# Kernel tuning notes

Hardware: AMD Instinct MI355X
Metric: run time of the kernel (lower is better)

Reference implementation:

```python
import jax, jax.numpy as jnp
import numpy as np

B, S, D = 4, 2048, 512
H, DK, DV = 8, 64, 64
EPS = 1e-6
MASK_FILL = -1e-9  # faithful to the original masked_fill value (NOT -inf)


def setup_inputs() -> dict:
    key = jax.random.key(0)
    ks = jax.random.split(key, 9)
    sc = 0.05
    return {
        "q": jax.random.normal(ks[0], (B, S, D), jnp.float32),
        "k": jax.random.normal(ks[1], (B, S, D), jnp.float32),
        "v": jax.random.normal(ks[2], (B, S, D), jnp.float32),
        "src_mask": jax.random.randint(ks[3], (B, S), 0, 2, jnp.int32),
        "Wq": jax.random.normal(ks[4], (D, H * DK), jnp.float32) * sc,
        "Wk": jax.random.normal(ks[5], (D, H * DK), jnp.float32) * sc,
        "Wv": jax.random.normal(ks[6], (D, H * DV), jnp.float32) * sc,
        "Wo": jax.random.normal(ks[7], (H * DV, D), jnp.float32) * sc,
        "gamma": jnp.ones((D,), jnp.float32),
        "beta": jnp.zeros((D,), jnp.float32),
    }


def reference(q, k, v, src_mask, Wq, Wk, Wv, Wo, gamma, beta):
    b, len_q, _ = q.shape
    residual = q
    # QKV projections -> [B, H, S, dk/dv]
    qh = (q @ Wq).reshape(b, len_q, H, DK).transpose(0, 2, 1, 3)
    kh = (k @ Wk).reshape(b, -1, H, DK).transpose(0, 2, 1, 3)
    vh = (v @ Wv).reshape(b, -1, H, DV).transpose(0, 2, 1, 3)
    # scores [B, H, S, S]
    attn = jnp.einsum('bhqd,bhkd->bhqk', qh, kh) / jnp.sqrt(jnp.float32(DK))
    # pairwise src mask: outer product of [B,S] mask, diagonal forced to 1
    sm = src_mask[:, :len_q].astype(jnp.float32)
    am = sm[:, :, None] * sm[:, None, :]               # [B, S, S]
    idx = jnp.arange(len_q)
    am = am.at[:, idx, idx].set(1.0)
    attn = jnp.where(am[:, None, :, :] == 0, MASK_FILL, attn)
    attn = jax.nn.softmax(attn, axis=-1)
    out = jnp.einsum('bhqk,bhkd->bhqd', attn, vh)      # [B, H, S, dv]
    out = out.transpose(0, 2, 1, 3).reshape(b, len_q, H * DV)
    out = out @ Wo + residual
    # LayerNorm(eps=1e-6)
    mu = jnp.mean(out, axis=-1, keepdims=True)
    var = jnp.var(out, axis=-1, keepdims=True)
    out = (out - mu) * jax.lax.rsqrt(var + EPS) * gamma + beta
    return out, attn
```

## Files before the change

### kernel.cpp

```cpp
#include <hip/hip_runtime.h>
#include <math.h>

#define B_ 4
#define S_ 2048
#define D_ 512
#define H_ 8
#define NEG_FILL (-1e-9f)

typedef __attribute__((ext_vector_type(8))) short bf16x8;
typedef __attribute__((ext_vector_type(4))) float f32x4;

#define MFMA16(A, Bm, C) __builtin_amdgcn_mfma_f32_16x16x32_bf16((A), (Bm), (C), 0, 0, 0)

__device__ __forceinline__ short f2b(float f) {
  union { float f; unsigned u; } x;
  x.f = f;
  unsigned r = x.u + 0x7fffu + ((x.u >> 16) & 1u);
  return (short)(r >> 16);
}

__global__ __launch_bounds__(256) void prep_wt(
    const float* __restrict__ Wq, const float* __restrict__ Wk,
    const float* __restrict__ Wv, const float* __restrict__ Wo,
    short* __restrict__ Wqt, short* __restrict__ Wkt,
    short* __restrict__ Wvt, short* __restrict__ Wot)
{
  const float* W; short* Wt;
  switch (blockIdx.z) {
    case 0: W = Wq; Wt = Wqt; break;
    case 1: W = Wk; Wt = Wkt; break;
    case 2: W = Wv; Wt = Wvt; break;
    default: W = Wo; Wt = Wot; break;
  }
  __shared__ float Ws[64 * 68];
  const int t = threadIdx.x;
  const int n0 = blockIdx.x * 64, k0 = blockIdx.y * 64;

  #pragma unroll
  for (int rep = 0; rep < 4; ++rep) {
    int e4 = rep * 256 + t;
    int r = e4 >> 4, c0 = (e4 & 15) * 4;
    *(float4*)&Ws[r * 68 + c0] = *(const float4*)&W[(size_t)(k0 + r) * 512 + n0 + c0];
  }
  __syncthreads();

  int rn = t >> 2;
  int kb = (t & 3) * 16;
  union { short s[8]; int4 v; } pk;
  #pragma unroll
  for (int half = 0; half < 2; ++half) {
    #pragma unroll
    for (int i = 0; i < 8; ++i)
      pk.s[i] = f2b(Ws[(kb + half * 8 + i) * 68 + rn]);
    *(int4*)&Wt[(size_t)(n0 + rn) * 512 + k0 + kb + half * 8] = pk.v;
  }
}

__global__ __launch_bounds__(256) void qkv_mfma(
    const float* __restrict__ q, const float* __restrict__ k, const float* __restrict__ v,
    const short* __restrict__ Wqt, const short* __restrict__ Wkt, const short* __restrict__ Wvt,
    short* __restrict__ qh, short* __restrict__ kh, short* __restrict__ vt)
{
  const int z = blockIdx.z;
  const float* X = (z == 0) ? q : (z == 1) ? k : v;
  const short* Wt = (z == 0) ? Wqt : (z == 1) ? Wkt : Wvt;

  __shared__ short Xs[64 * 72];
  __shared__ short Wsh[64 * 72];

  const int t = threadIdx.x;
  const int wave = t >> 6, lane = t & 63, quad = lane >> 4, l15 = lane & 15;
  const int tile_n = blockIdx.x * 64;
  const int tile_m = blockIdx.y * 64;

  f32x4 acc[4];
  #pragma unroll
  for (int nt = 0; nt < 4; ++nt) acc[nt] = (f32x4){0.f, 0.f, 0.f, 0.f};

  for (int k0 = 0; k0 < 512; k0 += 64) {
    __syncthreads();
    #pragma unroll
    for (int rep = 0; rep < 4; ++rep) {
      int e4 = rep * 256 + t;
      int row = e4 >> 4, c0 = (e4 & 15) * 4;
      float4 xv = *(const float4*)&X[(size_t)(tile_m + row) * 512 + k0 + c0];
      *(short4*)&Xs[row * 72 + c0] =
          make_short4(f2b(xv.x), f2b(xv.y), f2b(xv.z), f2b(xv.w));
    }
    #pragma unroll
    for (int rep = 0; rep < 2; ++rep) {
      int e = rep * 256 + t;
      int row = e >> 3, c0 = (e & 7) * 8;
      *(int4*)&Wsh[row * 72 + c0] = *(const int4*)&Wt[(size_t)(tile_n + row) * 512 + k0 + c0];
    }
    __syncthreads();
    #pragma unroll
    for (int ks = 0; ks < 2; ++ks) {
      bf16x8 af = *(bf16x8*)&Xs[(wave * 16 + l15) * 72 + ks * 32 + quad * 8];
      #pragma unroll
      for (int nt = 0; nt < 4; ++nt) {
        bf16x8 bfr = *(bf16x8*)&Wsh[(nt * 16 + l15) * 72 + ks * 32 + quad * 8];
        acc[nt] = MFMA16(af, bfr, acc[nt]);
      }
    }
  }

  const int h = tile_n >> 6;
  if (z < 2) {
    short* Y = (z == 0) ? qh : kh;
    #pragma unroll
    for (int nt = 0; nt < 4; ++nt) {
      int d = nt * 16 + l15;
      #pragma unroll
      for (int r = 0; r < 4; ++r) {
        int row = tile_m + wave * 16 + quad * 4 + r;
        int b = row >> 11, s = row & (S_ - 1);
        Y[(((size_t)(b * H_ + h)) * S_ + s) * 64 + d] = f2b(acc[nt][r]);
      }
    }
  } else {
    int row0 = tile_m + wave * 16 + quad * 4;
    int b = row0 >> 11, s0 = row0 & (S_ - 1);
    #pragma unroll
    for (int nt = 0; nt < 4; ++nt) {
      int d = nt * 16 + l15;
      short4 pk = make_short4(f2b(acc[nt][0]), f2b(acc[nt][1]),
                              f2b(acc[nt][2]), f2b(acc[nt][3]));
      *(short4*)&vt[(((size_t)(b * H_ + h)) * 64 + d) * S_ + s0] = pk;
    }
  }
}

__global__ __launch_bounds__(256) void attn_mfma(
    const short* __restrict__ qh, const short* __restrict__ kh,
    const short* __restrict__ vt, const int* __restrict__ src_mask,
    float* __restrict__ attn_out, short* __restrict__ ohb)
{
  const int t = threadIdx.x;
  const int wave = t >> 6, lane = t & 63, quad = lane >> 4, l15 = lane & 15;
  const int q0 = blockIdx.x * 64;
  const int bh = blockIdx.y, b = bh >> 3, h = bh & 7;

  __shared__ short Ks[64 * 72];
  __shared__ short Vs[64 * 72];
  __shared__ short Ps[64 * 72];
  __shared__ int smq[64], smk[64];

  #pragma unroll
  for (int rep = 0; rep < 2; ++rep) {
    int e = rep * 256 + t;
    int row = e >> 3, c0 = (e & 7) * 8;
    *(int4*)&Ps[row * 72 + c0] =
        *(const int4*)&qh[((size_t)bh * S_ + q0 + row) * 64 + c0];
  }
  if (t < 64) smq[t] = src_mask[b * S_ + q0 + t];
  __syncthreads();

  bf16x8 qf[2];
  #pragma unroll
  for (int ks = 0; ks < 2; ++ks)
    qf[ks] = *(bf16x8*)&Ps[(wave * 16 + l15) * 72 + ks * 32 + quad * 8];

  int rloc[4], mqr[4], qir[4];
  #pragma unroll
  for (int r = 0; r < 4; ++r) {
    rloc[r] = wave * 16 + quad * 4 + r;
    mqr[r] = smq[rloc[r]];
    qir[r] = q0 + rloc[r];
  }

  float rs[4] = {0.f, 0.f, 0.f, 0.f};
  for (int kt0 = 0; kt0 < S_; kt0 += 64) {
    __syncthreads();
    #pragma unroll
    for (int rep = 0; rep < 2; ++rep) {
      int e = rep * 256 + t;
      int row = e >> 3, c0 = (e & 7) * 8;
      *(int4*)&Ks[row * 72 + c0] =
          *(const int4*)&kh[((size_t)bh * S_ + kt0 + row) * 64 + c0];
    }
    if (t < 64) smk[t] = src_mask[b * S_ + kt0 + t];
    __syncthreads();

    #pragma unroll
    for (int nt = 0; nt < 4; ++nt) {
      f32x4 c = (f32x4){0.f, 0.f, 0.f, 0.f};
      #pragma unroll
      for (int ks = 0; ks < 2; ++ks) {
        bf16x8 kf = *(bf16x8*)&Ks[(nt * 16 + l15) * 72 + ks * 32 + quad * 8];
        c = MFMA16(qf[ks], kf, c);
      }
      int mk = smk[nt * 16 + l15];
      int kj = kt0 + nt * 16 + l15;
      #pragma unroll
      for (int r = 0; r < 4; ++r) {
        float ss = c[r] * 0.125f;
        bool keep = (mqr[r] & mk) || (qir[r] == kj);
        ss = keep ? ss : NEG_FILL;
        rs[r] += __expf(ss);
      }
    }
  }
  #pragma unroll
  for (int r = 0; r < 4; ++r) {
    float vsum = rs[r];
    vsum += __shfl_xor(vsum, 1);
    vsum += __shfl_xor(vsum, 2);
    vsum += __shfl_xor(vsum, 4);
    vsum += __shfl_xor(vsum, 8);
    rs[r] = 1.f / vsum;
  }

  f32x4 oacc[4];
  #pragma unroll
  for (int dt = 0; dt < 4; ++dt) oacc[dt] = (f32x4){0.f, 0.f, 0.f, 0.f};

  for (int kt0 = 0; kt0 < S_; kt0 += 64) {
    __syncthreads();
    #pragma unroll
    for (int rep = 0; rep < 2; ++rep) {
      int e = rep * 256 + t;
      int row = e >> 3, c0 = (e & 7) * 8;
      *(int4*)&Ks[row * 72 + c0] =
          *(const int4*)&kh[((size_t)bh * S_ + kt0 + row) * 64 + c0];
      *(int4*)&Vs[row * 72 + c0] =
          *(const int4*)&vt[((size_t)bh * 64 + row) * S_ + kt0 + c0];
    }
    if (t < 64) smk[t] = src_mask[b * S_ + kt0 + t];
    __syncthreads();

    #pragma unroll
    for (int nt = 0; nt < 4; ++nt) {
      f32x4 c = (f32x4){0.f, 0.f, 0.f, 0.f};
      #pragma unroll
      for (int ks = 0; ks < 2; ++ks) {
        bf16x8 kf = *(bf16x8*)&Ks[(nt * 16 + l15) * 72 + ks * 32 + quad * 8];
        c = MFMA16(qf[ks], kf, c);
      }
      int mk = smk[nt * 16 + l15];
      int kj = kt0 + nt * 16 + l15;
      #pragma unroll
      for (int r = 0; r < 4; ++r) {
        float ss = c[r] * 0.125f;
        bool keep = (mqr[r] & mk) || (qir[r] == kj);
        ss = keep ? ss : NEG_FILL;
        float p = __expf(ss) * rs[r];
        attn_out[((size_t)bh * S_ + q0 + rloc[r]) * S_ + kj] = p;
        Ps[rloc[r] * 72 + nt * 16 + l15] = f2b(p);
      }
    }
    __syncthreads();

    bf16x8 pf[2];
    #pragma unroll
    for (int ks = 0; ks < 2; ++ks)
      pf[ks] = *(bf16x8*)&Ps[(wave * 16 + l15) * 72 + ks * 32 + quad * 8];
    #pragma unroll
    for (int dt = 0; dt < 4; ++dt) {
      #pragma unroll
      for (int ks = 0; ks < 2; ++ks) {
        bf16x8 vf = *(bf16x8*)&Vs[(dt * 16 + l15) * 72 + ks * 32 + quad * 8];
        oacc[dt] = MFMA16(pf[ks], vf, oacc[dt]);
      }
    }
  }

  #pragma unroll
  for (int dt = 0; dt < 4; ++dt) {
    int d = h * 64 + dt * 16 + l15;
    #pragma unroll
    for (int r = 0; r < 4; ++r)
      ohb[((size_t)b * S_ + q0 + rloc[r]) * 512 + d] = f2b(oacc[dt][r]);
  }
}

__global__ __launch_bounds__(256) void out_mfma(
    const short* __restrict__ ohb, const short* __restrict__ Wot,
    const float* __restrict__ resid, float* __restrict__ out)
{
  __shared__ short Xs[64 * 72];
  __shared__ short Wsh[64 * 72];

  const int t = threadIdx.x;
  const int wave = t >> 6, lane = t & 63, quad = lane >> 4, l15 = lane & 15;
  const int tile_n = blockIdx.x * 64;
  const int tile_m = blockIdx.y * 64;

  f32x4 acc[4];
  #pragma unroll
  for (int nt = 0; nt < 4; ++nt) acc[nt] = (f32x4){0.f, 0.f, 0.f, 0.f};

  for (int k0 = 0; k0 < 512; k0 += 64) {
    __syncthreads();
    #pragma unroll
    for (int rep = 0; rep < 2; ++rep) {
      int e = rep * 256 + t;
      int row = e >> 3, c0 = (e & 7) * 8;
      *(int4*)&Xs[row * 72 + c0] = *(const int4*)&ohb[(size_t)(tile_m + row) * 512 + k0 + c0];
      *(int4*)&Wsh[row * 72 + c0] = *(const int4*)&Wot[(size_t)(tile_n + row) * 512 + k0 + c0];
    }
    __syncthreads();
    #pragma unroll
    for (int ks = 0; ks < 2; ++ks) {
      bf16x8 af = *(bf16x8*)&Xs[(wave * 16 + l15) * 72 + ks * 32 + quad * 8];
      #pragma unroll
      for (int nt = 0; nt < 4; ++nt) {
        bf16x8 bfr = *(bf16x8*)&Wsh[(nt * 16 + l15) * 72 + ks * 32 + quad * 8];
        acc[nt] = MFMA16(af, bfr, acc[nt]);
      }
    }
  }

  #pragma unroll
  for (int nt = 0; nt < 4; ++nt) {
    int c = tile_n + nt * 16 + l15;
    #pragma unroll
    for (int r = 0; r < 4; ++r) {
      size_t row = tile_m + wave * 16 + quad * 4 + r;
      out[row * 512 + c] = acc[nt][r] + resid[row * 512 + c];
    }
  }
}

__global__ __launch_bounds__(256) void ln_kernel(
    float* __restrict__ io, const float* __restrict__ gamma, const float* __restrict__ beta)
{
  const int wid  = threadIdx.x >> 6;
  const int lane = threadIdx.x & 63;
  const size_t row = (size_t)blockIdx.x * 4 + wid;
  const size_t base = row * 512 + lane * 8;

  float4 x0 = *(const float4*)&io[base];
  float4 x1 = *(const float4*)&io[base + 4];
  float xs[8] = {x0.x, x0.y, x0.z, x0.w, x1.x, x1.y, x1.z, x1.w};

  float s = 0.f, s2 = 0.f;
  #pragma unroll
  for (int i = 0; i < 8; ++i) { s += xs[i]; s2 = fmaf(xs[i], xs[i], s2); }
  #pragma unroll
  for (int m = 1; m < 64; m <<= 1) {
    s  += __shfl_xor(s, m);
    s2 += __shfl_xor(s2, m);
  }
  float mu  = s * (1.f / 512.f);
  float var = s2 * (1.f / 512.f) - mu * mu;
  float rsq = rsqrtf(var + 1e-6f);

  float4 g0 = *(const float4*)&gamma[lane * 8];
  float4 g1 = *(const float4*)&gamma[lane * 8 + 4];
  float4 b0 = *(const float4*)&beta[lane * 8];
  float4 b1 = *(const float4*)&beta[lane * 8 + 4];
  float gs[8] = {g0.x, g0.y, g0.z, g0.w, g1.x, g1.y, g1.z, g1.w};
  float bs[8] = {b0.x, b0.y, b0.z, b0.w, b1.x, b1.y, b1.z, b1.w};

  float ys[8];
  #pragma unroll
  for (int i = 0; i < 8; ++i) ys[i] = (xs[i] - mu) * rsq * gs[i] + bs[i];
  *(float4*)&io[base]     = make_float4(ys[0], ys[1], ys[2], ys[3]);
  *(float4*)&io[base + 4] = make_float4(ys[4], ys[5], ys[6], ys[7]);
}

extern "C" void kernel_launch(void* const* d_in, const int* in_sizes, int n_in,
                              void* d_out, int out_size, void* d_ws, size_t ws_size,
                              hipStream_t stream)
{
  const float* q     = (const float*)d_in[0];
  const float* k     = (const float*)d_in[1];
  const float* v     = (const float*)d_in[2];
  const int*  smask  = (const int*)d_in[3];
  const float* Wq    = (const float*)d_in[4];
  const float* Wk    = (const float*)d_in[5];
  const float* Wv    = (const float*)d_in[6];
  const float* Wo    = (const float*)d_in[7];
  const float* gamma = (const float*)d_in[8];
  const float* beta  = (const float*)d_in[9];

  float* out  = (float*)d_out;
  float* attn = out + (size_t)B_ * S_ * D_;

  short* wsS = (short*)d_ws;
  short* qh  = wsS;
  short* kh  = qh + 4194304;
  short* vt  = kh + 4194304;
  short* ohb = vt + 4194304;
  short* Wqt = ohb + 4194304;
  short* Wkt = Wqt + 262144;
  short* Wvt = Wkt + 262144;
  short* Wot = Wvt + 262144;

  prep_wt<<<dim3(8, 8, 4), 256, 0, stream>>>(Wq, Wk, Wv, Wo, Wqt, Wkt, Wvt, Wot);
  qkv_mfma<<<dim3(8, 128, 3), 256, 0, stream>>>(q, k, v, Wqt, Wkt, Wvt, qh, kh, vt);
  attn_mfma<<<dim3(32, 32), 256, 0, stream>>>(qh, kh, vt, smask, attn, ohb);
  out_mfma<<<dim3(8, 128), 256, 0, stream>>>(ohb, Wot, q, out);
  ln_kernel<<<2048, 256, 0, stream>>>(out, gamma, beta);
}
```

Measured before the change: 804.3 us.

## Simplify attention masking arithmetically, fold score scale into Q, widen GEMM tiles

```diff
diff --git a/kernel.cpp b/kernel.cpp
--- a/kernel.cpp
+++ b/kernel.cpp
@@ -5,7 +5,6 @@
 #define S_ 2048
 #define D_ 512
 #define H_ 8
-#define NEG_FILL (-1e-9f)
 
 typedef __attribute__((ext_vector_type(8))) short bf16x8;
 typedef __attribute__((ext_vector_type(4))) float f32x4;
@@ -66,16 +65,16 @@
   const short* Wt = (z == 0) ? Wqt : (z == 1) ? Wkt : Wvt;
 
   __shared__ short Xs[64 * 72];
-  __shared__ short Wsh[64 * 72];
+  __shared__ short Wsh[128 * 72];
 
   const int t = threadIdx.x;
   const int wave = t >> 6, lane = t & 63, quad = lane >> 4, l15 = lane & 15;
-  const int tile_n = blockIdx.x * 64;
+  const int tile_n = blockIdx.x * 128;
   const int tile_m = blockIdx.y * 64;
 
-  f32x4 acc[4];
-  #pragma unroll
-  for (int nt = 0; nt < 4; ++nt) acc[nt] = (f32x4){0.f, 0.f, 0.f, 0.f};
+  f32x4 acc[8];
+  #pragma unroll
+  for (int nt = 0; nt < 8; ++nt) acc[nt] = (f32x4){0.f, 0.f, 0.f, 0.f};
 
   for (int k0 = 0; k0 < 512; k0 += 64) {
     __syncthreads();
@@ -88,7 +87,7 @@
           make_short4(f2b(xv.x), f2b(xv.y), f2b(xv.z), f2b(xv.w));
     }
     #pragma unroll
-    for (int rep = 0; rep < 2; ++rep) {
+    for (int rep = 0; rep < 4; ++rep) {
       int e = rep * 256 + t;
       int row = e >> 3, c0 = (e & 7) * 8;
       *(int4*)&Wsh[row * 72 + c0] = *(const int4*)&Wt[(size_t)(tile_n + row) * 512 + k0 + c0];
@@ -98,35 +97,37 @@
     for (int ks = 0; ks < 2; ++ks) {
       bf16x8 af = *(bf16x8*)&Xs[(wave * 16 + l15) * 72 + ks * 32 + quad * 8];
       #pragma unroll
-      for (int nt = 0; nt < 4; ++nt) {
+      for (int nt = 0; nt < 8; ++nt) {
         bf16x8 bfr = *(bf16x8*)&Wsh[(nt * 16 + l15) * 72 + ks * 32 + quad * 8];
         acc[nt] = MFMA16(af, bfr, acc[nt]);
       }
     }
   }
 
-  const int h = tile_n >> 6;
+  const float scale = (z == 0) ? 0.125f : 1.0f;
   if (z < 2) {
     short* Y = (z == 0) ? qh : kh;
     #pragma unroll
-    for (int nt = 0; nt < 4; ++nt) {
-      int d = nt * 16 + l15;
+    for (int nt = 0; nt < 8; ++nt) {
+      int d = tile_n + nt * 16 + l15;
+      int h = d >> 6, dd = d & 63;
       #pragma unroll
       for (int r = 0; r < 4; ++r) {
         int row = tile_m + wave * 16 + quad * 4 + r;
         int b = row >> 11, s = row & (S_ - 1);
-        Y[(((size_t)(b * H_ + h)) * S_ + s) * 64 + d] = f2b(acc[nt][r]);
+        Y[(((size_t)(b * H_ + h)) * S_ + s) * 64 + dd] = f2b(acc[nt][r] * scale);
       }
     }
   } else {
     int row0 = tile_m + wave * 16 + quad * 4;
     int b = row0 >> 11, s0 = row0 & (S_ - 1);
     #pragma unroll
-    for (int nt = 0; nt < 4; ++nt) {
-      int d = nt * 16 + l15;
+    for (int nt = 0; nt < 8; ++nt) {
+      int d = tile_n + nt * 16 + l15;
+      int h = d >> 6, dd = d & 63;
       short4 pk = make_short4(f2b(acc[nt][0]), f2b(acc[nt][1]),
                               f2b(acc[nt][2]), f2b(acc[nt][3]));
-      *(short4*)&vt[(((size_t)(b * H_ + h)) * 64 + d) * S_ + s0] = pk;
+      *(short4*)&vt[(((size_t)(b * H_ + h)) * 64 + dd) * S_ + s0] = pk;
     }
   }
 }
@@ -144,7 +145,7 @@
   __shared__ short Ks[64 * 72];
   __shared__ short Vs[64 * 72];
   __shared__ short Ps[64 * 72];
-  __shared__ int smq[64], smk[64];
+  __shared__ float smqf[64], smkf[64];
 
   #pragma unroll
   for (int rep = 0; rep < 2; ++rep) {
@@ -153,7 +154,7 @@
     *(int4*)&Ps[row * 72 + c0] =
         *(const int4*)&qh[((size_t)bh * S_ + q0 + row) * 64 + c0];
   }
-  if (t < 64) smq[t] = src_mask[b * S_ + q0 + t];
+  if (t < 64) smqf[t] = (float)src_mask[b * S_ + q0 + t];
   __syncthreads();
 
   bf16x8 qf[2];
@@ -161,15 +162,15 @@
   for (int ks = 0; ks < 2; ++ks)
     qf[ks] = *(bf16x8*)&Ps[(wave * 16 + l15) * 72 + ks * 32 + quad * 8];
 
-  int rloc[4], mqr[4], qir[4];
+  int rloc[4];
+  float mqf[4];
   #pragma unroll
   for (int r = 0; r < 4; ++r) {
     rloc[r] = wave * 16 + quad * 4 + r;
-    mqr[r] = smq[rloc[r]];
-    qir[r] = q0 + rloc[r];
-  }
-
-  float rs[4] = {0.f, 0.f, 0.f, 0.f};
+    mqf[r] = smqf[rloc[r]];
+  }
+
+  float rs[4] = {128.f, 128.f, 128.f, 128.f};
   for (int kt0 = 0; kt0 < S_; kt0 += 64) {
     __syncthreads();
     #pragma unroll
@@ -179,9 +180,10 @@
       *(int4*)&Ks[row * 72 + c0] =
           *(const int4*)&kh[((size_t)bh * S_ + kt0 + row) * 64 + c0];
     }
-    if (t < 64) smk[t] = src_mask[b * S_ + kt0 + t];
-    __syncthreads();
-
+    if (t < 64) smkf[t] = (float)src_mask[b * S_ + kt0 + t];
+    __syncthreads();
+
+    const bool diagtile = (kt0 == q0);
     #pragma unroll
     for (int nt = 0; nt < 4; ++nt) {
       f32x4 c = (f32x4){0.f, 0.f, 0.f, 0.f};
@@ -190,14 +192,23 @@
         bf16x8 kf = *(bf16x8*)&Ks[(nt * 16 + l15) * 72 + ks * 32 + quad * 8];
         c = MFMA16(qf[ks], kf, c);
       }
-      int mk = smk[nt * 16 + l15];
-      int kj = kt0 + nt * 16 + l15;
-      #pragma unroll
-      for (int r = 0; r < 4; ++r) {
-        float ss = c[r] * 0.125f;
-        bool keep = (mqr[r] & mk) || (qir[r] == kj);
-        ss = keep ? ss : NEG_FILL;
-        rs[r] += __expf(ss);
+      float mk = smkf[nt * 16 + l15];
+      if (diagtile && nt == wave) {
+        #pragma unroll
+        for (int r = 0; r < 4; ++r) {
+          float e = __expf(c[r]);
+          float mm = mqf[r] * mk;
+          float pun = fmaf(mm, e - 1.f, 1.f);
+          if (l15 == quad * 4 + r) pun = e;
+          rs[r] += pun - 1.f;
+        }
+      } else {
+        #pragma unroll
+        for (int r = 0; r < 4; ++r) {
+          float e = __expf(c[r]);
+          float mm = mqf[r] * mk;
+          rs[r] = fmaf(mm, e - 1.f, rs[r]);
+        }
       }
     }
   }
@@ -215,6 +226,11 @@
   #pragma unroll
   for (int dt = 0; dt < 4; ++dt) oacc[dt] = (f32x4){0.f, 0.f, 0.f, 0.f};
 
+  float* arow[4];
+  #pragma unroll
+  for (int r = 0; r < 4; ++r)
+    arow[r] = attn_out + ((size_t)bh * S_ + q0 + rloc[r]) * S_;
+
   for (int kt0 = 0; kt0 < S_; kt0 += 64) {
     __syncthreads();
     #pragma unroll
@@ -226,9 +242,10 @@
       *(int4*)&Vs[row * 72 + c0] =
           *(const int4*)&vt[((size_t)bh * 64 + row) * S_ + kt0 + c0];
     }
-    if (t < 64) smk[t] = src_mask[b * S_ + kt0 + t];
-    __syncthreads();
-
+    if (t < 64) smkf[t] = (float)src_mask[b * S_ + kt0 + t];
+    __syncthreads();
+
+    const bool diagtile = (kt0 == q0);
     #pragma unroll
     for (int nt = 0; nt < 4; ++nt) {
       f32x4 c = (f32x4){0.f, 0.f, 0.f, 0.f};
@@ -237,16 +254,29 @@
         bf16x8 kf = *(bf16x8*)&Ks[(nt * 16 + l15) * 72 + ks * 32 + quad * 8];
         c = MFMA16(qf[ks], kf, c);
       }
-      int mk = smk[nt * 16 + l15];
+      float mk = smkf[nt * 16 + l15];
       int kj = kt0 + nt * 16 + l15;
-      #pragma unroll
-      for (int r = 0; r < 4; ++r) {
-        float ss = c[r] * 0.125f;
-        bool keep = (mqr[r] & mk) || (qir[r] == kj);
-        ss = keep ? ss : NEG_FILL;
-        float p = __expf(ss) * rs[r];
-        attn_out[((size_t)bh * S_ + q0 + rloc[r]) * S_ + kj] = p;
-        Ps[rloc[r] * 72 + nt * 16 + l15] = f2b(p);
+      if (diagtile && nt == wave) {
+        #pragma unroll
+        for (int r = 0; r < 4; ++r) {
+          float e = __expf(c[r]);
+          float mm = mqf[r] * mk;
+          float pun = fmaf(mm, e - 1.f, 1.f);
+          if (l15 == quad * 4 + r) pun = e;
+          float p = pun * rs[r];
+          arow[r][kj] = p;
+          Ps[rloc[r] * 72 + nt * 16 + l15] = f2b(p);
+        }
+      } else {
+        #pragma unroll
+        for (int r = 0; r < 4; ++r) {
+          float e = __expf(c[r]);
+          float mm = mqf[r] * mk;
+          float pun = fmaf(mm, e - 1.f, 1.f);
+          float p = pun * rs[r];
+          arow[r][kj] = p;
+          Ps[rloc[r] * 72 + nt * 16 + l15] = f2b(p);
+        }
       }
     }
     __syncthreads();
@@ -279,16 +309,16 @@
     const float* __restrict__ resid, float* __restrict__ out)
 {
   __shared__ short Xs[64 * 72];
-  __shared__ short Wsh[64 * 72];
+  __shared__ short Wsh[128 * 72];
 
   const int t = threadIdx.x;
   const int wave = t >> 6, lane = t & 63, quad = lane >> 4, l15 = lane & 15;
-  const int tile_n = blockIdx.x * 64;
+  const int tile_n = blockIdx.x * 128;
   const int tile_m = blockIdx.y * 64;
 
-  f32x4 acc[4];
-  #pragma unroll
-  for (int nt = 0; nt < 4; ++nt) acc[nt] = (f32x4){0.f, 0.f, 0.f, 0.f};
+  f32x4 acc[8];
+  #pragma unroll
+  for (int nt = 0; nt < 8; ++nt) acc[nt] = (f32x4){0.f, 0.f, 0.f, 0.f};
 
   for (int k0 = 0; k0 < 512; k0 += 64) {
     __syncthreads();
@@ -297,6 +327,11 @@
       int e = rep * 256 + t;
       int row = e >> 3, c0 = (e & 7) * 8;
       *(int4*)&Xs[row * 72 + c0] = *(const int4*)&ohb[(size_t)(tile_m + row) * 512 + k0 + c0];
+    }
+    #pragma unroll
+    for (int rep = 0; rep < 4; ++rep) {
+      int e = rep * 256 + t;
+      int row = e >> 3, c0 = (e & 7) * 8;
       *(int4*)&Wsh[row * 72 + c0] = *(const int4*)&Wot[(size_t)(tile_n + row) * 512 + k0 + c0];
     }
     __syncthreads();
@@ -304,7 +339,7 @@
     for (int ks = 0; ks < 2; ++ks) {
       bf16x8 af = *(bf16x8*)&Xs[(wave * 16 + l15) * 72 + ks * 32 + quad * 8];
       #pragma unroll
-      for (int nt = 0; nt < 4; ++nt) {
+      for (int nt = 0; nt < 8; ++nt) {
         bf16x8 bfr = *(bf16x8*)&Wsh[(nt * 16 + l15) * 72 + ks * 32 + quad * 8];
         acc[nt] = MFMA16(af, bfr, acc[nt]);
       }
@@ -312,7 +347,7 @@
   }
 
   #pragma unroll
-  for (int nt = 0; nt < 4; ++nt) {
+  for (int nt = 0; nt < 8; ++nt) {
     int c = tile_n + nt * 16 + l15;
     #pragma unroll
     for (int r = 0; r < 4; ++r) {
@@ -389,8 +424,8 @@
   short* Wot = Wvt + 262144;
 
   prep_wt<<<dim3(8, 8, 4), 256, 0, stream>>>(Wq, Wk, Wv, Wo, Wqt, Wkt, Wvt, Wot);
-  qkv_mfma<<<dim3(8, 128, 3), 256, 0, stream>>>(q, k, v, Wqt, Wkt, Wvt, qh, kh, vt);
+  qkv_mfma<<<dim3(4, 128, 3), 256, 0, stream>>>(q, k, v, Wqt, Wkt, Wvt, qh, kh, vt);
   attn_mfma<<<dim3(32, 32), 256, 0, stream>>>(qh, kh, vt, smask, attn, ohb);
-  out_mfma<<<dim3(8, 128), 256, 0, stream>>>(ohb, Wot, q, out);
+  out_mfma<<<dim3(4, 128), 256, 0, stream>>>(ohb, Wot, q, out);
   ln_kernel<<<2048, 256, 0, stream>>>(out, gamma, beta);
 }
```

Result: slower. 835.1 us (+3.8%).
